# Performance work log

Hardware: AMD Instinct MI355X
Metric: run time of the kernel (lower is better)

The kernel has to match this reference:

```python
import jax, jax.numpy as jnp
import numpy as np

NUM_COLORS = 10
COLOR_MAPPING_W = 0.4
CONSISTENCY_W = 0.3
RULE_W = 0.2
EXACT_BONUS = 5.0


def _color_rules(targets, num_colors):
    # Vectorized equivalent of per-batch torch.unique(): sorted unique colors
    # of each grid written into the first slots of a [B, 10] rules tensor.
    B = targets.shape[0]
    colors = jnp.arange(num_colors)
    presence = jnp.any(targets[:, :, :, None] == colors, axis=(1, 2))  # [B, 10]
    pos = jnp.cumsum(presence.astype(jnp.int32), axis=1) - 1           # slot index per color
    cols = jnp.where(presence, pos, num_colors)                        # absent -> dump slot
    rules = jnp.zeros((B, num_colors + 1), dtype=jnp.float32)
    rules = rules.at[jnp.arange(B)[:, None], cols].set(
        colors.astype(jnp.float32) * presence.astype(jnp.float32))
    return rules[:, :num_colors]


def setup_inputs() -> dict:
    key = jax.random.key(0)
    k1, k2, k3, k4 = jax.random.split(key, 4)
    B, C, H, W = 4096, NUM_COLORS, 30, 30
    return {
        "color_output": jax.random.normal(k1, (B, C, H, W), dtype=jnp.float32),
        "targets": jax.random.randint(k2, (B, H, W), 0, C),
        "color_attention": jax.random.uniform(k3, (B, H, W, C), dtype=jnp.float32),
        "lstm_rules": jax.random.normal(k4, (B, C), dtype=jnp.float32),
    }


def reference(color_output, targets, color_attention, lstm_rules):
    B, C, H, W = color_output.shape
    # exact-match cross entropy (mean over B*H*W)
    logp = jax.nn.log_softmax(color_output, axis=1)               # [B,C,H,W]
    ce = -jnp.take_along_axis(logp, targets[:, None], axis=1).mean()
    pred_colors = jnp.argmax(color_output, axis=1)                # [B,H,W]
    eq = (pred_colors == targets).astype(jnp.float32)
    exact_count = eq.sum()
    # color mapping: MSE(attention, one_hot(targets))
    onehot = jax.nn.one_hot(targets, C, dtype=jnp.float32)        # [B,H,W,C]
    color_mapping = jnp.mean((color_attention - onehot) ** 2)
    # sliding 2x2 window consistency, fused: avg over windows of (1 - mean eq)
    s = eq[:, :-1, :-1] + eq[:, 1:, :-1] + eq[:, :-1, 1:] + eq[:, 1:, 1:]
    consistency = 1.0 - s.mean() / 4.0
    # rule learning: MSE against per-batch sorted-unique-color rules
    rule_target = _color_rules(targets, C)
    rule_loss = jnp.mean((lstm_rules - rule_target) ** 2)
    total = (ce + COLOR_MAPPING_W * color_mapping
             + CONSISTENCY_W * consistency + RULE_W * rule_loss)
    total = total - (exact_count / B) * EXACT_BONUS  # bonus is 0 when count is 0
    total = jnp.maximum(total, 0.001)
    return (total, ce, color_mapping, consistency, rule_loss, exact_count)
```

## Files before the change

### kernel.cpp

```cpp
#include <hip/hip_runtime.h>


namespace {
constexpr int kB = 4096;
constexpr int kC = 10;
constexpr int kH = 30;
constexpr int kW = 30;
constexpr int kHW = kH * kW;
constexpr int kCHW = kC * kHW;
constexpr int kThreads = 256;
constexpr int kP4 = kHW / 4;
constexpr int kF4 = kCHW / 4;
}

__global__ __launch_bounds__(kThreads, 4) void iris_main(
    const float* __restrict__ logits_g,
    const int* __restrict__ targets_g,
    const float* __restrict__ att_g,
    const float* __restrict__ rules_g,
    float* __restrict__ ce_part,
    float* __restrict__ cm_part,
    unsigned* __restrict__ weq_part,
    unsigned* __restrict__ eq_part,
    float* __restrict__ rule_part)
{
    const int b = blockIdx.x;
    const int tid = threadIdx.x;
    const float* __restrict__ logits = logits_g + (size_t)b * kCHW;
    const int* __restrict__ tgt = targets_g + (size_t)b * kHW;
    const float* __restrict__ att = att_g + (size_t)b * kCHW;

    float ce_acc = 0.f, cm_acc = 0.f;
    unsigned weq_acc = 0u, eq_acc = 0u, mask_acc = 0u;

    const bool owner = (tid < kP4);
    const int p0 = tid * 4;

    int ta[4] = {0, 0, 0, 0};
    float x[kC][4];
    float atg[4] = {0.f, 0.f, 0.f, 0.f};
    if (owner) {
        const int4 tv = *reinterpret_cast<const int4*>(tgt + p0);
        ta[0] = tv.x; ta[1] = tv.y; ta[2] = tv.z; ta[3] = tv.w;
#pragma unroll
        for (int c = 0; c < kC; ++c) {
            const float4 v = *reinterpret_cast<const float4*>(logits + c * kHW + p0);
            x[c][0] = v.x; x[c][1] = v.y; x[c][2] = v.z; x[c][3] = v.w;
        }
        mask_acc = (1u << ta[0]) | (1u << ta[1]) | (1u << ta[2]) | (1u << ta[3]);
#pragma unroll
        for (int j = 0; j < 4; ++j)
            atg[j] = att[(p0 + j) * kC + ta[j]];
    }
    __builtin_amdgcn_sched_barrier(0);

    {
        float sq = 0.f;
#pragma unroll
        for (int k = 0; k < 8; ++k) {
            const float4 v = *reinterpret_cast<const float4*>(att + 4 * (tid + kThreads * k));
            sq += v.x * v.x + v.y * v.y + v.z * v.z + v.w * v.w;
        }
        if (tid < kF4 - 8 * kThreads) {
            const float4 v = *reinterpret_cast<const float4*>(att + 4 * (tid + kThreads * 8));
            sq += v.x * v.x + v.y * v.y + v.z * v.z + v.w * v.w;
        }
        cm_acc = sq;
    }

    if (owner) {
        cm_acc -= 2.f * (atg[0] + atg[1] + atg[2] + atg[3]);

        float xm[4], xt[4];
        int am[4];
#pragma unroll
        for (int j = 0; j < 4; ++j) { xm[j] = -3.4e38f; xt[j] = 0.f; am[j] = 0; }
#pragma unroll
        for (int c = 0; c < kC; ++c) {
#pragma unroll
            for (int j = 0; j < 4; ++j) {
                const bool gt = x[c][j] > xm[j];
                am[j] = gt ? c : am[j];
                xm[j] = gt ? x[c][j] : xm[j];
                xt[j] = (c == ta[j]) ? x[c][j] : xt[j];
            }
        }
#pragma unroll
        for (int j = 0; j < 4; ++j) {
            float s = 0.f;
#pragma unroll
            for (int c = 0; c < kC; ++c) s += __expf(x[c][j] - xm[j]);
            ce_acc += xm[j] + __logf(s) - xt[j];

            const unsigned eq = (am[j] == ta[j]) ? 1u : 0u;
            eq_acc += eq;
            const int p = p0 + j;
            const int h = p / kW;
            const int w = p - h * kW;
            const unsigned wgt = ((h == 0 || h == kH - 1) ? 1u : 2u) *
                                 ((w == 0 || w == kW - 1) ? 1u : 2u);
            weq_acc += eq * wgt;
        }
    }

#pragma unroll
    for (int off = 32; off > 0; off >>= 1) {
        ce_acc  += __shfl_down(ce_acc, off);
        cm_acc  += __shfl_down(cm_acc, off);
        weq_acc += __shfl_down(weq_acc, off);
        eq_acc  += __shfl_down(eq_acc, off);
        mask_acc |= __shfl_down(mask_acc, off);
    }

    __shared__ float s_ce[4], s_cm[4];
    __shared__ unsigned s_weq[4], s_eq[4], s_mask[4];
    const int wave = tid >> 6;
    if ((tid & 63) == 0) {
        s_ce[wave] = ce_acc;
        s_cm[wave] = cm_acc;
        s_weq[wave] = weq_acc;
        s_eq[wave] = eq_acc;
        s_mask[wave] = mask_acc;
    }
    __syncthreads();

    if (tid == 0) {
        ce_part[b]  = s_ce[0] + s_ce[1] + s_ce[2] + s_ce[3];
        cm_part[b]  = s_cm[0] + s_cm[1] + s_cm[2] + s_cm[3];
        weq_part[b] = s_weq[0] + s_weq[1] + s_weq[2] + s_weq[3];
        eq_part[b]  = s_eq[0] + s_eq[1] + s_eq[2] + s_eq[3];
        const unsigned mask = s_mask[0] | s_mask[1] | s_mask[2] | s_mask[3];

        const float* __restrict__ lr = rules_g + (size_t)b * kC;
        unsigned mrem = mask;
        float rl = 0.f;
#pragma unroll
        for (int s2 = 0; s2 < kC; ++s2) {
            float v = 0.f;
            if (mrem) {
                v = (float)(__ffs(mrem) - 1);
                mrem &= mrem - 1u;
            }
            const float d = lr[s2] - v;
            rl += d * d;
        }
        rule_part[b] = rl;
    }
}

__global__ __launch_bounds__(1024) void iris_finalize(
    const float* __restrict__ ce_part,
    const float* __restrict__ cm_part,
    const unsigned* __restrict__ weq_part,
    const unsigned* __restrict__ eq_part,
    const float* __restrict__ rule_part,
    float* __restrict__ out)
{
    const int tid = threadIdx.x;
    double ce = 0.0, cm = 0.0, rl = 0.0;
    unsigned long long weq = 0ull, eqc = 0ull;
#pragma unroll
    for (int k = 0; k < 4; ++k) {
        const int i = tid + 1024 * k;
        ce += (double)ce_part[i];
        cm += (double)cm_part[i];
        rl += (double)rule_part[i];
        weq += (unsigned long long)weq_part[i];
        eqc += (unsigned long long)eq_part[i];
    }
#pragma unroll
    for (int off = 32; off > 0; off >>= 1) {
        ce  += __shfl_down(ce, off);
        cm  += __shfl_down(cm, off);
        rl  += __shfl_down(rl, off);
        weq += __shfl_down(weq, off);
        eqc += __shfl_down(eqc, off);
    }
    __shared__ double sd[3][16];
    __shared__ unsigned long long su[2][16];
    const int wave = tid >> 6;
    if ((tid & 63) == 0) {
        sd[0][wave] = ce; sd[1][wave] = cm; sd[2][wave] = rl;
        su[0][wave] = weq; su[1][wave] = eqc;
    }
    __syncthreads();
    if (tid == 0) {
        ce = 0.0; cm = 0.0; rl = 0.0; weq = 0ull; eqc = 0ull;
#pragma unroll
        for (int i = 0; i < 16; ++i) {
            ce += sd[0][i]; cm += sd[1][i]; rl += sd[2][i];
            weq += su[0][i]; eqc += su[1][i];
        }
        const double ce_m = ce / ((double)kB * kHW);
        const double cm_m = (cm + (double)kB * kHW) / ((double)kB * kHW * kC);
        const double s_mean = (double)weq / ((double)kB * (kH - 1) * (kW - 1));
        const double cons = 1.0 - s_mean / 4.0;
        const double rl_m = rl / ((double)kB * kC);
        const double exact = (double)eqc;
        double total = ce_m + 0.4 * cm_m + 0.3 * cons + 0.2 * rl_m
                       - (exact / (double)kB) * 5.0;
        if (total < 0.001) total = 0.001;
        out[0] = (float)total;
        out[1] = (float)ce_m;
        out[2] = (float)cm_m;
        out[3] = (float)cons;
        out[4] = (float)rl_m;
        out[5] = (float)exact;
    }
}

extern "C" void kernel_launch(void* const* d_in, const int* in_sizes, int n_in,
                              void* d_out, int out_size, void* d_ws, size_t ws_size,
                              hipStream_t stream) {
    const float* color_output    = (const float*)d_in[0];
    const int*   targets         = (const int*)d_in[1];
    const float* color_attention = (const float*)d_in[2];
    const float* lstm_rules      = (const float*)d_in[3];
    float* out = (float*)d_out;

    float*    ce_part   = (float*)d_ws;
    float*    cm_part   = ce_part + kB;
    unsigned* weq_part  = (unsigned*)(cm_part + kB);
    unsigned* eq_part   = weq_part + kB;
    float*    rule_part = (float*)(eq_part + kB);

    iris_main<<<kB, kThreads, 0, stream>>>(color_output, targets, color_attention,
                                           lstm_rules, ce_part, cm_part,
                                           weq_part, eq_part, rule_part);
    iris_finalize<<<1, 1024, 0, stream>>>(ce_part, cm_part, weq_part, eq_part,
                                          rule_part, out);
}
```

Baseline: 315.9 us.

## Stage logits through LDS with fully coalesced loads and prefetch rules early

Logits for each batch are now loaded cooperatively by all 256 threads as contiguous float4s into a 36 KB LDS buffer, instead of having only 225 owner threads load strided per-channel float4s into registers. The owner threads then read their channel values back from LDS twice, once for the max/argmax pass and once for the exp-sum pass, which lowers register pressure. Thread 0 also prefetches the lstm_rules row at the start to hide its latency. The trade-offs are an added __syncthreads, extra LDS traffic, and dropping the 4-waves-per-EU occupancy hint, since the large LDS allocation limits how many blocks fit on a CU.

```diff
diff --git a/kernel.cpp b/kernel.cpp
--- a/kernel.cpp
+++ b/kernel.cpp
@@ -13,7 +13,7 @@
 constexpr int kF4 = kCHW / 4;
 }
 
-__global__ __launch_bounds__(kThreads, 4) void iris_main(
+__global__ __launch_bounds__(kThreads) void iris_main(
     const float* __restrict__ logits_g,
     const int* __restrict__ targets_g,
     const float* __restrict__ att_g,
@@ -24,6 +24,10 @@
     unsigned* __restrict__ eq_part,
     float* __restrict__ rule_part)
 {
+    __shared__ float lds_x[kCHW];
+    __shared__ float s_ce[4], s_cm[4];
+    __shared__ unsigned s_weq[4], s_eq[4], s_mask[4];
+
     const int b = blockIdx.x;
     const int tid = threadIdx.x;
     const float* __restrict__ logits = logits_g + (size_t)b * kCHW;
@@ -36,21 +40,38 @@
     const bool owner = (tid < kP4);
     const int p0 = tid * 4;
 
+    float lr[kC];
+    if (tid == 0) {
+#pragma unroll
+        for (int c = 0; c < kC; c += 2) {
+            const float2 v = *reinterpret_cast<const float2*>(rules_g + (size_t)b * kC + c);
+            lr[c] = v.x; lr[c + 1] = v.y;
+        }
+    }
+
     int ta[4] = {0, 0, 0, 0};
-    float x[kC][4];
-    float atg[4] = {0.f, 0.f, 0.f, 0.f};
     if (owner) {
         const int4 tv = *reinterpret_cast<const int4*>(tgt + p0);
         ta[0] = tv.x; ta[1] = tv.y; ta[2] = tv.z; ta[3] = tv.w;
-#pragma unroll
-        for (int c = 0; c < kC; ++c) {
-            const float4 v = *reinterpret_cast<const float4*>(logits + c * kHW + p0);
-            x[c][0] = v.x; x[c][1] = v.y; x[c][2] = v.z; x[c][3] = v.w;
-        }
         mask_acc = (1u << ta[0]) | (1u << ta[1]) | (1u << ta[2]) | (1u << ta[3]);
-#pragma unroll
-        for (int j = 0; j < 4; ++j)
-            atg[j] = att[(p0 + j) * kC + ta[j]];
+    }
+
+#pragma unroll
+    for (int k = 0; k < 8; ++k) {
+        const int f4 = tid + kThreads * k;
+        const float4 v = *reinterpret_cast<const float4*>(logits + 4 * f4);
+        *reinterpret_cast<float4*>(lds_x + 4 * f4) = v;
+    }
+    if (tid < kF4 - 8 * kThreads) {
+        const int f4 = tid + kThreads * 8;
+        const float4 v = *reinterpret_cast<const float4*>(logits + 4 * f4);
+        *reinterpret_cast<float4*>(lds_x + 4 * f4) = v;
+    }
+
+    float atg[4] = {0.f, 0.f, 0.f, 0.f};
+    if (owner) {
+#pragma unroll
+        for (int j = 0; j < 4; ++j) atg[j] = att[(p0 + j) * kC + ta[j]];
     }
     __builtin_amdgcn_sched_barrier(0);
 
@@ -68,6 +89,8 @@
         cm_acc = sq;
     }
 
+    __syncthreads();
+
     if (owner) {
         cm_acc -= 2.f * (atg[0] + atg[1] + atg[2] + atg[3]);
 
@@ -77,21 +100,28 @@
         for (int j = 0; j < 4; ++j) { xm[j] = -3.4e38f; xt[j] = 0.f; am[j] = 0; }
 #pragma unroll
         for (int c = 0; c < kC; ++c) {
+            const float4 v = *reinterpret_cast<const float4*>(lds_x + c * kHW + p0);
+            const float xv[4] = {v.x, v.y, v.z, v.w};
 #pragma unroll
             for (int j = 0; j < 4; ++j) {
-                const bool gt = x[c][j] > xm[j];
+                const bool gt = xv[j] > xm[j];
                 am[j] = gt ? c : am[j];
-                xm[j] = gt ? x[c][j] : xm[j];
-                xt[j] = (c == ta[j]) ? x[c][j] : xt[j];
+                xm[j] = gt ? xv[j] : xm[j];
+                xt[j] = (c == ta[j]) ? xv[j] : xt[j];
             }
         }
+        float s[4] = {0.f, 0.f, 0.f, 0.f};
+#pragma unroll
+        for (int c = 0; c < kC; ++c) {
+            const float4 v = *reinterpret_cast<const float4*>(lds_x + c * kHW + p0);
+            s[0] += __expf(v.x - xm[0]);
+            s[1] += __expf(v.y - xm[1]);
+            s[2] += __expf(v.z - xm[2]);
+            s[3] += __expf(v.w - xm[3]);
+        }
 #pragma unroll
         for (int j = 0; j < 4; ++j) {
-            float s = 0.f;
-#pragma unroll
-            for (int c = 0; c < kC; ++c) s += __expf(x[c][j] - xm[j]);
-            ce_acc += xm[j] + __logf(s) - xt[j];
-
+            ce_acc += xm[j] + __logf(s[j]) - xt[j];
             const unsigned eq = (am[j] == ta[j]) ? 1u : 0u;
             eq_acc += eq;
             const int p = p0 + j;
@@ -111,9 +141,6 @@
         eq_acc  += __shfl_down(eq_acc, off);
         mask_acc |= __shfl_down(mask_acc, off);
     }
-
-    __shared__ float s_ce[4], s_cm[4];
-    __shared__ unsigned s_weq[4], s_eq[4], s_mask[4];
     const int wave = tid >> 6;
     if ((tid & 63) == 0) {
         s_ce[wave] = ce_acc;
@@ -131,7 +158,6 @@
         eq_part[b]  = s_eq[0] + s_eq[1] + s_eq[2] + s_eq[3];
         const unsigned mask = s_mask[0] | s_mask[1] | s_mask[2] | s_mask[3];
 
-        const float* __restrict__ lr = rules_g + (size_t)b * kC;
         unsigned mrem = mask;
         float rl = 0.f;
 #pragma unroll
```

Result: no change. 316.9 us (+0.3%).

## Split fused loss kernel into grid-stride attention, CE, and rules kernels

Applied to the files above, without the earlier changes.

Replaces the one-block-per-batch fused kernel with three kernels. The first is a grid-stride sum of squares over the attention tensor. The second is a grid-stride CE/argmax pass that uses an online softmax. The third computes the per-batch color mask for the rule loss. The aim is to remove idle lanes (only 225 of 256 threads owned pixels) and the high register pressure from buffering ten logits per pixel, and to give better streaming of the large attention tensor. In exchange it adds kernel launches and re-reads targets, and the online softmax needs extra exponentials per element.

```diff
diff --git a/kernel.cpp b/kernel.cpp
--- a/kernel.cpp
+++ b/kernel.cpp
@@ -8,129 +8,121 @@
 constexpr int kW = 30;
 constexpr int kHW = kH * kW;
 constexpr int kCHW = kC * kHW;
+constexpr int kQuadsPerB = kHW / 4;
+constexpr int kQuads = kB * kQuadsPerB;
+constexpr int kAttF4 = kB * kCHW / 4;
+constexpr int kGrid = 2048;
 constexpr int kThreads = 256;
-constexpr int kP4 = kHW / 4;
-constexpr int kF4 = kCHW / 4;
-}
-
-__global__ __launch_bounds__(kThreads, 4) void iris_main(
+constexpr int kStride = kGrid * kThreads;
+}
+
+__global__ __launch_bounds__(kThreads) void iris_att_sq(
+    const float* __restrict__ att_g, float* __restrict__ cmsq_part) {
+    const int tid = threadIdx.x;
+    float sq = 0.f;
+    for (int idx = blockIdx.x * kThreads + tid; idx < kAttF4; idx += kStride) {
+        const float4 v = reinterpret_cast<const float4*>(att_g)[idx];
+        sq += v.x * v.x + v.y * v.y + v.z * v.z + v.w * v.w;
+    }
+#pragma unroll
+    for (int off = 32; off > 0; off >>= 1) sq += __shfl_down(sq, off);
+    __shared__ float s[4];
+    if ((tid & 63) == 0) s[tid >> 6] = sq;
+    __syncthreads();
+    if (tid == 0) cmsq_part[blockIdx.x] = s[0] + s[1] + s[2] + s[3];
+}
+
+__global__ __launch_bounds__(kThreads) void iris_ce(
     const float* __restrict__ logits_g,
     const int* __restrict__ targets_g,
     const float* __restrict__ att_g,
-    const float* __restrict__ rules_g,
     float* __restrict__ ce_part,
-    float* __restrict__ cm_part,
+    float* __restrict__ cmat_part,
     unsigned* __restrict__ weq_part,
-    unsigned* __restrict__ eq_part,
-    float* __restrict__ rule_part)
+    unsigned* __restrict__ eq_part)
 {
-    const int b = blockIdx.x;
     const int tid = threadIdx.x;
-    const float* __restrict__ logits = logits_g + (size_t)b * kCHW;
-    const int* __restrict__ tgt = targets_g + (size_t)b * kHW;
-    const float* __restrict__ att = att_g + (size_t)b * kCHW;
-
-    float ce_acc = 0.f, cm_acc = 0.f;
-    unsigned weq_acc = 0u, eq_acc = 0u, mask_acc = 0u;
-
-    const bool owner = (tid < kP4);
-    const int p0 = tid * 4;
-
-    int ta[4] = {0, 0, 0, 0};
-    float x[kC][4];
-    float atg[4] = {0.f, 0.f, 0.f, 0.f};
-    if (owner) {
-        const int4 tv = *reinterpret_cast<const int4*>(tgt + p0);
-        ta[0] = tv.x; ta[1] = tv.y; ta[2] = tv.z; ta[3] = tv.w;
+    float ce_acc = 0.f, at_acc = 0.f;
+    unsigned weq_acc = 0u, eq_acc = 0u;
+
+    for (int q = blockIdx.x * kThreads + tid; q < kQuads; q += kStride) {
+        const int b = q / kQuadsPerB;
+        const int i = q - b * kQuadsPerB;
+        const int p0 = 4 * i;
+
+        const int4 tv = *reinterpret_cast<const int4*>(targets_g + (size_t)b * kHW + p0);
+        const int ta[4] = {tv.x, tv.y, tv.z, tv.w};
+
+        const float* __restrict__ ap = att_g + (size_t)b * kCHW + (size_t)p0 * kC;
+        at_acc += ap[0 * kC + ta[0]] + ap[1 * kC + ta[1]] +
+                  ap[2 * kC + ta[2]] + ap[3 * kC + ta[3]];
+
+        const float* __restrict__ lg = logits_g + (size_t)b * kCHW + p0;
+        float m[4], s[4], xt[4];
+        int am[4];
+#pragma unroll
+        for (int j = 0; j < 4; ++j) { m[j] = -3.4e38f; s[j] = 0.f; xt[j] = 0.f; am[j] = 0; }
 #pragma unroll
         for (int c = 0; c < kC; ++c) {
-            const float4 v = *reinterpret_cast<const float4*>(logits + c * kHW + p0);
-            x[c][0] = v.x; x[c][1] = v.y; x[c][2] = v.z; x[c][3] = v.w;
-        }
-        mask_acc = (1u << ta[0]) | (1u << ta[1]) | (1u << ta[2]) | (1u << ta[3]);
-#pragma unroll
-        for (int j = 0; j < 4; ++j)
-            atg[j] = att[(p0 + j) * kC + ta[j]];
-    }
-    __builtin_amdgcn_sched_barrier(0);
-
-    {
-        float sq = 0.f;
-#pragma unroll
-        for (int k = 0; k < 8; ++k) {
-            const float4 v = *reinterpret_cast<const float4*>(att + 4 * (tid + kThreads * k));
-            sq += v.x * v.x + v.y * v.y + v.z * v.z + v.w * v.w;
-        }
-        if (tid < kF4 - 8 * kThreads) {
-            const float4 v = *reinterpret_cast<const float4*>(att + 4 * (tid + kThreads * 8));
-            sq += v.x * v.x + v.y * v.y + v.z * v.z + v.w * v.w;
-        }
-        cm_acc = sq;
-    }
-
-    if (owner) {
-        cm_acc -= 2.f * (atg[0] + atg[1] + atg[2] + atg[3]);
-
-        float xm[4], xt[4];
-        int am[4];
-#pragma unroll
-        for (int j = 0; j < 4; ++j) { xm[j] = -3.4e38f; xt[j] = 0.f; am[j] = 0; }
-#pragma unroll
-        for (int c = 0; c < kC; ++c) {
+            const float4 v = *reinterpret_cast<const float4*>(lg + c * kHW);
+            const float xv[4] = {v.x, v.y, v.z, v.w};
 #pragma unroll
             for (int j = 0; j < 4; ++j) {
-                const bool gt = x[c][j] > xm[j];
+                const bool gt = xv[j] > m[j];
+                const float mn = gt ? xv[j] : m[j];
+                s[j] = s[j] * __expf(m[j] - mn) + __expf(xv[j] - mn);
+                m[j] = mn;
                 am[j] = gt ? c : am[j];
-                xm[j] = gt ? x[c][j] : xm[j];
-                xt[j] = (c == ta[j]) ? x[c][j] : xt[j];
+                xt[j] = (c == ta[j]) ? xv[j] : xt[j];
             }
         }
 #pragma unroll
         for (int j = 0; j < 4; ++j) {
-            float s = 0.f;
-#pragma unroll
-            for (int c = 0; c < kC; ++c) s += __expf(x[c][j] - xm[j]);
-            ce_acc += xm[j] + __logf(s) - xt[j];
-
+            ce_acc += m[j] + __logf(s[j]) - xt[j];
             const unsigned eq = (am[j] == ta[j]) ? 1u : 0u;
             eq_acc += eq;
             const int p = p0 + j;
             const int h = p / kW;
             const int w = p - h * kW;
-            const unsigned wgt = ((h == 0 || h == kH - 1) ? 1u : 2u) *
-                                 ((w == 0 || w == kW - 1) ? 1u : 2u);
-            weq_acc += eq * wgt;
+            weq_acc += eq * (((h == 0 || h == kH - 1) ? 1u : 2u) *
+                             ((w == 0 || w == kW - 1) ? 1u : 2u));
         }
     }
 
 #pragma unroll
     for (int off = 32; off > 0; off >>= 1) {
         ce_acc  += __shfl_down(ce_acc, off);
-        cm_acc  += __shfl_down(cm_acc, off);
+        at_acc  += __shfl_down(at_acc, off);
         weq_acc += __shfl_down(weq_acc, off);
         eq_acc  += __shfl_down(eq_acc, off);
-        mask_acc |= __shfl_down(mask_acc, off);
-    }
-
-    __shared__ float s_ce[4], s_cm[4];
-    __shared__ unsigned s_weq[4], s_eq[4], s_mask[4];
+    }
+    __shared__ float sf[2][4];
+    __shared__ unsigned su[2][4];
     const int wave = tid >> 6;
     if ((tid & 63) == 0) {
-        s_ce[wave] = ce_acc;
-        s_cm[wave] = cm_acc;
-        s_weq[wave] = weq_acc;
-        s_eq[wave] = eq_acc;
-        s_mask[wave] = mask_acc;
+        sf[0][wave] = ce_acc; sf[1][wave] = at_acc;
+        su[0][wave] = weq_acc; su[1][wave] = eq_acc;
     }
     __syncthreads();
-
     if (tid == 0) {
-        ce_part[b]  = s_ce[0] + s_ce[1] + s_ce[2] + s_ce[3];
-        cm_part[b]  = s_cm[0] + s_cm[1] + s_cm[2] + s_cm[3];
-        weq_part[b] = s_weq[0] + s_weq[1] + s_weq[2] + s_weq[3];
-        eq_part[b]  = s_eq[0] + s_eq[1] + s_eq[2] + s_eq[3];
-        const unsigned mask = s_mask[0] | s_mask[1] | s_mask[2] | s_mask[3];
-
+        ce_part[blockIdx.x]   = sf[0][0] + sf[0][1] + sf[0][2] + sf[0][3];
+        cmat_part[blockIdx.x] = sf[1][0] + sf[1][1] + sf[1][2] + sf[1][3];
+        weq_part[blockIdx.x]  = su[0][0] + su[0][1] + su[0][2] + su[0][3];
+        eq_part[blockIdx.x]   = su[1][0] + su[1][1] + su[1][2] + su[1][3];
+    }
+}
+
+__global__ __launch_bounds__(64) void iris_rules(
+    const int* __restrict__ targets_g, const float* __restrict__ rules_g,
+    float* __restrict__ rule_part) {
+    const int b = blockIdx.x;
+    const int lane = threadIdx.x;
+    const int* __restrict__ tgt = targets_g + (size_t)b * kHW;
+    unsigned mask = 0u;
+    for (int k = lane; k < kHW; k += 64) mask |= 1u << tgt[k];
+#pragma unroll
+    for (int off = 32; off > 0; off >>= 1) mask |= __shfl_down(mask, off);
+    if (lane == 0) {
         const float* __restrict__ lr = rules_g + (size_t)b * kC;
         unsigned mrem = mask;
         float rl = 0.f;
@@ -150,49 +142,53 @@
 
 __global__ __launch_bounds__(1024) void iris_finalize(
     const float* __restrict__ ce_part,
-    const float* __restrict__ cm_part,
+    const float* __restrict__ cmat_part,
+    const float* __restrict__ cmsq_part,
     const unsigned* __restrict__ weq_part,
     const unsigned* __restrict__ eq_part,
     const float* __restrict__ rule_part,
-    float* __restrict__ out)
-{
+    float* __restrict__ out) {
     const int tid = threadIdx.x;
-    double ce = 0.0, cm = 0.0, rl = 0.0;
+    double ce = 0.0, cma = 0.0, cms = 0.0, rl = 0.0;
     unsigned long long weq = 0ull, eqc = 0ull;
 #pragma unroll
-    for (int k = 0; k < 4; ++k) {
+    for (int k = 0; k < 2; ++k) {
         const int i = tid + 1024 * k;
-        ce += (double)ce_part[i];
-        cm += (double)cm_part[i];
-        rl += (double)rule_part[i];
+        ce  += (double)ce_part[i];
+        cma += (double)cmat_part[i];
+        cms += (double)cmsq_part[i];
         weq += (unsigned long long)weq_part[i];
         eqc += (unsigned long long)eq_part[i];
     }
 #pragma unroll
+    for (int k = 0; k < 4; ++k) rl += (double)rule_part[tid + 1024 * k];
+#pragma unroll
     for (int off = 32; off > 0; off >>= 1) {
         ce  += __shfl_down(ce, off);
-        cm  += __shfl_down(cm, off);
+        cma += __shfl_down(cma, off);
+        cms += __shfl_down(cms, off);
         rl  += __shfl_down(rl, off);
         weq += __shfl_down(weq, off);
         eqc += __shfl_down(eqc, off);
     }
-    __shared__ double sd[3][16];
+    __shared__ double sd[4][16];
     __shared__ unsigned long long su[2][16];
     const int wave = tid >> 6;
     if ((tid & 63) == 0) {
-        sd[0][wave] = ce; sd[1][wave] = cm; sd[2][wave] = rl;
+        sd[0][wave] = ce; sd[1][wave] = cma; sd[2][wave] = cms; sd[3][wave] = rl;
         su[0][wave] = weq; su[1][wave] = eqc;
     }
     __syncthreads();
     if (tid == 0) {
-        ce = 0.0; cm = 0.0; rl = 0.0; weq = 0ull; eqc = 0ull;
+        ce = 0.0; cma = 0.0; cms = 0.0; rl = 0.0; weq = 0ull; eqc = 0ull;
 #pragma unroll
         for (int i = 0; i < 16; ++i) {
-            ce += sd[0][i]; cm += sd[1][i]; rl += sd[2][i];
+            ce += sd[0][i]; cma += sd[1][i]; cms += sd[2][i]; rl += sd[3][i];
             weq += su[0][i]; eqc += su[1][i];
         }
-        const double ce_m = ce / ((double)kB * kHW);
-        const double cm_m = (cm + (double)kB * kHW) / ((double)kB * kHW * kC);
+        const double npix = (double)kB * kHW;
+        const double ce_m = ce / npix;
+        const double cm_m = (cms - 2.0 * cma + npix) / (npix * kC);
         const double s_mean = (double)weq / ((double)kB * (kH - 1) * (kW - 1));
         const double cons = 1.0 - s_mean / 4.0;
         const double rl_m = rl / ((double)kB * kC);
@@ -219,14 +215,16 @@
     float* out = (float*)d_out;
 
     float*    ce_part   = (float*)d_ws;
-    float*    cm_part   = ce_part + kB;
-    unsigned* weq_part  = (unsigned*)(cm_part + kB);
-    unsigned* eq_part   = weq_part + kB;
-    float*    rule_part = (float*)(eq_part + kB);
-
-    iris_main<<<kB, kThreads, 0, stream>>>(color_output, targets, color_attention,
-                                           lstm_rules, ce_part, cm_part,
-                                           weq_part, eq_part, rule_part);
-    iris_finalize<<<1, 1024, 0, stream>>>(ce_part, cm_part, weq_part, eq_part,
-                                          rule_part, out);
-}
+    float*    cmat_part = ce_part + kGrid;
+    float*    cmsq_part = cmat_part + kGrid;
+    unsigned* weq_part  = (unsigned*)(cmsq_part + kGrid);
+    unsigned* eq_part   = weq_part + kGrid;
+    float*    rule_part = (float*)(eq_part + kGrid);
+
+    iris_att_sq<<<kGrid, kThreads, 0, stream>>>(color_attention, cmsq_part);
+    iris_ce<<<kGrid, kThreads, 0, stream>>>(color_output, targets, color_attention,
+                                            ce_part, cmat_part, weq_part, eq_part);
+    iris_rules<<<kB, 64, 0, stream>>>(targets, lstm_rules, rule_part);
+    iris_finalize<<<1, 1024, 0, stream>>>(ce_part, cmat_part, cmsq_part,
+                                          weq_part, eq_part, rule_part, out);
+}
```

Result: slower. 329.3 us (+4.2%).
